# Performance work log

Hardware: AMD Instinct MI355X
Metric: run time of the kernel (lower is better)

The kernel has to match this reference:

```python
import jax, jax.numpy as jnp
import numpy as np

N_NODES = 16000
N_EDGES = 256000
DIM = 256
HEADS = 8
DH = DIM // HEADS
BLOCKS = 3
EPS = 1e-5


def _ln_graph(x, g, b):
    # PyG LayerNorm, mode='graph', batch=None: scalar mean/std over ALL elements,
    # then per-channel affine.
    x = x - x.mean()
    x = x / (x.std() + EPS)
    return x * g + b


def _block(x, src, dst, x_edge, inv_dist, p):
    (Wq, bq, Wk, bk, Wv, bv, We, Ws, bs, g1, b1, W1, c1, W2, c2, g2, b2) = p
    # per-edge gather + projections  [E, H, DH]
    q = (x[dst] @ Wq + bq).reshape(N_EDGES, HEADS, DH)
    e = (x_edge @ We).reshape(N_EDGES, HEADS, DH)          # lin_edge (no bias)
    k = (x[src] @ Wk + bk).reshape(N_EDGES, HEADS, DH) + e
    # distance-scaled attention logits [E, H]
    alpha = (q * k).sum(-1) * (inv_dist[:, None] / np.sqrt(DH))
    # segment softmax over destination nodes (PyG softmax, +1e-16 in denom)
    amax = jax.ops.segment_max(alpha, dst, num_segments=N_NODES)
    ex = jnp.exp(alpha - amax[dst])
    denom = jax.ops.segment_sum(ex, dst, num_segments=N_NODES)
    attn = ex / (denom[dst] + 1e-16)
    v = (x[src] @ Wv + bv).reshape(N_EDGES, HEADS, DH) + e
    msg = (v * attn[:, :, None]).reshape(N_EDGES, DIM)      # concat heads
    out = jax.ops.segment_sum(msg, dst, num_segments=N_NODES)
    out = out + x @ Ws + bs                                 # root / skip weight
    x = _ln_graph(x + out, g1, b1)                          # mha residual + norm
    ffn = jnp.maximum(x @ W1 + c1, 0.0) @ W2 + c2           # 2-layer ReLU MLP
    return _ln_graph(x + ffn, g2, b2)


def setup_inputs() -> dict:
    key = jax.random.key(0)
    ks = jax.random.split(key, 16)
    s = 0.05
    B = BLOCKS

    def w(k, shape):
        return jax.random.normal(k, shape, jnp.float32) * s

    return {
        'x': jax.random.normal(ks[0], (N_NODES, DIM), jnp.float32),
        'edge_index': jax.random.randint(ks[1], (2, N_EDGES), 0, N_NODES),
        'x_edge': jax.random.normal(ks[2], (N_EDGES, DIM), jnp.float32),
        'x_dist': jax.random.uniform(ks[3], (N_EDGES,), jnp.float32, 1.0, 5.0),
        'Wq': w(ks[4], (B, DIM, DIM)), 'bq': jnp.zeros((B, DIM), jnp.float32),
        'Wk': w(ks[5], (B, DIM, DIM)), 'bk': jnp.zeros((B, DIM), jnp.float32),
        'Wv': w(ks[6], (B, DIM, DIM)), 'bv': jnp.zeros((B, DIM), jnp.float32),
        'We': w(ks[7], (B, DIM, DIM)),
        'Wskip': w(ks[8], (B, DIM, DIM)), 'bskip': jnp.zeros((B, DIM), jnp.float32),
        'ln1_g': jnp.ones((B, DIM), jnp.float32), 'ln1_b': jnp.zeros((B, DIM), jnp.float32),
        'W1': w(ks[9], (B, DIM, 4 * DIM)), 'bf1': jnp.zeros((B, 4 * DIM), jnp.float32),
        'W2': w(ks[10], (B, 4 * DIM, DIM)), 'bf2': jnp.zeros((B, DIM), jnp.float32),
        'ln2_g': jnp.ones((B, DIM), jnp.float32), 'ln2_b': jnp.zeros((B, DIM), jnp.float32),
    }


def reference(x, edge_index, x_edge, x_dist, Wq, bq, Wk, bk, Wv, bv, We,
              Wskip, bskip, ln1_g, ln1_b, W1, bf1, W2, bf2, ln2_g, ln2_b):
    src, dst = edge_index[0], edge_index[1]  # PyG: x_j = x[src], x_i = x[dst]
    inv_dist = 1.0 / x_dist
    for i in range(BLOCKS):
        p = (Wq[i], bq[i], Wk[i], bk[i], Wv[i], bv[i], We[i], Wskip[i], bskip[i],
             ln1_g[i], ln1_b[i], W1[i], bf1[i], W2[i], bf2[i], ln2_g[i], ln2_b[i])
        x = _block(x, src, dst, x_edge, inv_dist, p)
    return x
```

## Files before the change

### kernel.cpp

```cpp
#include <hip/hip_runtime.h>
#include <hip/hip_bf16.h>
#include <cstddef>

#define N_NODES 16000
#define N_EDGES 256000
#define DIM 256
#define HEADS 8
#define DFF 1024
#define LN_EPS 1e-5f
#define CNT ((float)((size_t)N_NODES * DIM))
#define RSDH 0.17677669529663687f

typedef __attribute__((ext_vector_type(8))) short short8;
typedef __attribute__((ext_vector_type(4))) float floatx4;

__device__ __forceinline__ float bf2f(unsigned int s) {
    return __uint_as_float(s << 16);
}

__device__ __forceinline__ float2 ln_ms(const float* __restrict__ s) {
    float mu = s[0] * (1.0f / CNT);
    float var = s[1] * (1.0f / CNT) - mu * mu;
    float2 r; r.x = mu; r.y = 1.0f / (sqrtf(fmaxf(var, 0.0f)) + LN_EPS);
    return r;
}

__device__ __forceinline__ void async16(const __hip_bfloat16* g, __hip_bfloat16* l) {
    __builtin_amdgcn_global_load_lds(
        (const __attribute__((address_space(1))) void*)g,
        (__attribute__((address_space(3))) void*)l, 16, 0, 0);
}

__device__ __forceinline__ void pack8(__hip_bfloat16* d, float4 a, float4 b) {
    union { short8 f; __hip_bfloat16 h[8]; } u;
    u.h[0] = __float2bfloat16(a.x); u.h[1] = __float2bfloat16(a.y);
    u.h[2] = __float2bfloat16(a.z); u.h[3] = __float2bfloat16(a.w);
    u.h[4] = __float2bfloat16(b.x); u.h[5] = __float2bfloat16(b.y);
    u.h[6] = __float2bfloat16(b.z); u.h[7] = __float2bfloat16(b.w);
    *(short8*)d = u.f;
}

template<int BIAS, int RELU, int RES, int OBF16, int ACVT>
__global__ __launch_bounds__(256) void mgemm_k(
    const void* __restrict__ Ap, const __hip_bfloat16* __restrict__ Bt,
    const float* __restrict__ bias, const float* __restrict__ res,
    void* __restrict__ C, int M, int K, int N,
    const float* __restrict__ lnA_s, const float* __restrict__ lnA_g,
    const float* __restrict__ lnA_b,
    const float* __restrict__ lnR_s, const float* __restrict__ lnR_g,
    const float* __restrict__ lnR_b,
    float* __restrict__ ostats)
{
    __shared__ __hip_bfloat16 As[128 * 32];
    __shared__ __hip_bfloat16 Bs[128 * 32];
    __shared__ float rs[8];
    const int tid = threadIdx.x;
    const int lane = tid & 63, wv = tid >> 6;
    const int wm = (wv & 1) * 64, wn = (wv >> 1) * 64;
    const int row0 = blockIdx.y * 128, col0 = blockIdx.x * 128;
    const int lr = tid >> 2;
    const int lk = (tid & 3) * 8;

    float muA = 0.0f, scA = 1.0f;
    if (ACVT && lnA_s) { float2 t = ln_ms(lnA_s); muA = t.x; scA = t.y; }

    floatx4 acc[4][4];
    const floatx4 zf = {0.f, 0.f, 0.f, 0.f};
    #pragma unroll
    for (int i = 0; i < 4; i++)
        #pragma unroll
        for (int j = 0; j < 4; j++) acc[i][j] = zf;

    const int a_fo = (wm + (lane & 15)) * 32 + (lane >> 4) * 8;
    const int b_fo = (wn + (lane & 15)) * 32 + (lane >> 4) * 8;

    for (int k0 = 0; k0 < K; k0 += 32) {
        if (ACVT) {
            const float* A = (const float*)Ap;
            const float* p0 = A + (size_t)(row0 + lr) * K + k0 + lk;
            const float* p1 = A + (size_t)(row0 + lr + 64) * K + k0 + lk;
            float4 v0 = *(const float4*)(p0);
            float4 v1 = *(const float4*)(p0 + 4);
            float4 w0 = *(const float4*)(p1);
            float4 w1 = *(const float4*)(p1 + 4);
            if (lnA_s) {
                float4 ga = *(const float4*)(lnA_g + k0 + lk);
                float4 gb = *(const float4*)(lnA_g + k0 + lk + 4);
                float4 ba = *(const float4*)(lnA_b + k0 + lk);
                float4 bb = *(const float4*)(lnA_b + k0 + lk + 4);
                v0.x = (v0.x - muA) * scA * ga.x + ba.x;
                v0.y = (v0.y - muA) * scA * ga.y + ba.y;
                v0.z = (v0.z - muA) * scA * ga.z + ba.z;
                v0.w = (v0.w - muA) * scA * ga.w + ba.w;
                v1.x = (v1.x - muA) * scA * gb.x + bb.x;
                v1.y = (v1.y - muA) * scA * gb.y + bb.y;
                v1.z = (v1.z - muA) * scA * gb.z + bb.z;
                v1.w = (v1.w - muA) * scA * gb.w + bb.w;
                w0.x = (w0.x - muA) * scA * ga.x + ba.x;
                w0.y = (w0.y - muA) * scA * ga.y + ba.y;
                w0.z = (w0.z - muA) * scA * ga.z + ba.z;
                w0.w = (w0.w - muA) * scA * ga.w + ba.w;
                w1.x = (w1.x - muA) * scA * gb.x + bb.x;
                w1.y = (w1.y - muA) * scA * gb.y + bb.y;
                w1.z = (w1.z - muA) * scA * gb.z + bb.z;
                w1.w = (w1.w - muA) * scA * gb.w + bb.w;
            }
            pack8(As + tid * 8, v0, v1);
            pack8(As + 2048 + tid * 8, w0, w1);
        } else {
            const __hip_bfloat16* A = (const __hip_bfloat16*)Ap;
            async16(A + (size_t)(row0 + lr) * K + k0 + lk, As + tid * 8);
            async16(A + (size_t)(row0 + lr + 64) * K + k0 + lk, As + 2048 + tid * 8);
        }
        async16(Bt + (size_t)(col0 + lr) * K + k0 + lk, Bs + tid * 8);
        async16(Bt + (size_t)(col0 + lr + 64) * K + k0 + lk, Bs + 2048 + tid * 8);
        __syncthreads();
        short8 a[4], b[4];
        #pragma unroll
        for (int i = 0; i < 4; i++) {
            a[i] = *(const short8*)(As + a_fo + i * 16 * 32);
            b[i] = *(const short8*)(Bs + b_fo + i * 16 * 32);
        }
        #pragma unroll
        for (int i = 0; i < 4; i++)
            #pragma unroll
            for (int j = 0; j < 4; j++)
                acc[i][j] = __builtin_amdgcn_mfma_f32_16x16x32_bf16(a[i], b[j], acc[i][j], 0, 0, 0);
        __syncthreads();
    }
    float muR = 0.0f, scR = 1.0f;
    if (RES && lnR_s) { float2 t = ln_ms(lnR_s); muR = t.x; scR = t.y; }
    const int rbase = row0 + wm + (lane >> 4) * 4;
    const int cbase = col0 + wn + (lane & 15);
    float s1 = 0.0f, s2 = 0.0f;
    #pragma unroll
    for (int j = 0; j < 4; j++) {
        const int c = cbase + j * 16;
        float bb = BIAS ? bias[c] : 0.0f;
        float gr = (RES && lnR_s) ? lnR_g[c] : 1.0f;
        float br = (RES && lnR_s) ? lnR_b[c] : 0.0f;
        #pragma unroll
        for (int i = 0; i < 4; i++) {
            #pragma unroll
            for (int r = 0; r < 4; r++) {
                const int rr = rbase + i * 16 + r;
                float v = acc[i][j][r] + bb;
                if (RELU) v = fmaxf(v, 0.0f);
                if (RES) {
                    float rv = res[(size_t)rr * N + c];
                    if (lnR_s) rv = (rv - muR) * scR * gr + br;
                    v += rv;
                }
                if (ostats) { s1 += v; s2 += v * v; }
                if (OBF16) ((__hip_bfloat16*)C)[(size_t)rr * N + c] = __float2bfloat16(v);
                else       ((float*)C)[(size_t)rr * N + c] = v;
            }
        }
    }
    if (ostats) {
        #pragma unroll
        for (int o = 32; o > 0; o >>= 1) {
            s1 += __shfl_down(s1, o);
            s2 += __shfl_down(s2, o);
        }
        if (lane == 0) { rs[wv] = s1; rs[4 + wv] = s2; }
        __syncthreads();
        if (tid == 0) {
            atomicAdd(&ostats[0], rs[0] + rs[1] + rs[2] + rs[3]);
            atomicAdd(&ostats[1], rs[4] + rs[5] + rs[6] + rs[7]);
        }
    }
}

__global__ __launch_bounds__(256) void tcvt_k(const float* __restrict__ src,
                                              __hip_bfloat16* __restrict__ dst,
                                              int R, int C)
{
    __shared__ float t[32][33];
    const int c0 = blockIdx.x * 32, r0 = blockIdx.y * 32;
    const int tx = threadIdx.x & 31, ty = threadIdx.x >> 5;
    #pragma unroll
    for (int j = 0; j < 32; j += 8)
        t[ty + j][tx] = src[(size_t)(r0 + ty + j) * C + c0 + tx];
    __syncthreads();
    #pragma unroll
    for (int j = 0; j < 32; j += 8)
        dst[(size_t)(c0 + ty + j) * R + r0 + tx] = __float2bfloat16(t[tx][ty + j]);
}

__global__ __launch_bounds__(256) void bcat_k(const float* __restrict__ bq,
                                              const float* __restrict__ bk,
                                              const float* __restrict__ bv,
                                              const float* __restrict__ bs,
                                              float* __restrict__ o)
{
    int t = blockIdx.x * 256 + threadIdx.x;
    float v = (t < 256) ? bq[t] : (t < 512) ? bk[t - 256]
            : (t < 768) ? bv[t - 512] : bs[t - 768];
    o[t] = v;
}

__global__ __launch_bounds__(256) void hist_k(const int* __restrict__ dst, int* __restrict__ deg)
{
    int e = blockIdx.x * blockDim.x + threadIdx.x;
    if (e < N_EDGES) atomicAdd(&deg[dst[e]], 1);
}

__global__ __launch_bounds__(1024) void scan_k(const int* __restrict__ deg,
                                               int* __restrict__ rowptr,
                                               int* __restrict__ cursor)
{
    __shared__ int wsum[16];
    const int t = threadIdx.x;
    const int base = t * 16;
    int local[16];
    int s = 0;
    if (t < 1000) {
        #pragma unroll
        for (int j = 0; j < 16; j++) { local[j] = s; s += deg[base + j]; }
    }
    const int lane = t & 63, w = t >> 6;
    int v = s;
    #pragma unroll
    for (int off = 1; off < 64; off <<= 1) {
        int u = __shfl_up(v, off);
        if (lane >= off) v += u;
    }
    if (lane == 63) wsum[w] = v;
    __syncthreads();
    if (t == 0) {
        int r = 0;
        #pragma unroll
        for (int i = 0; i < 16; i++) { int u = wsum[i]; wsum[i] = r; r += u; }
    }
    __syncthreads();
    const int excl = v - s + wsum[w];
    if (t < 1000) {
        #pragma unroll
        for (int j = 0; j < 16; j++) {
            rowptr[base + j] = excl + local[j];
            cursor[base + j] = excl + local[j];
        }
        if (t == 999) rowptr[16000] = excl + s;
    }
}

__global__ __launch_bounds__(256) void scatter_k(const int* __restrict__ dst,
                                                 const int* __restrict__ src,
                                                 const float* __restrict__ xd,
                                                 int* __restrict__ cursor,
                                                 int* __restrict__ eperm,
                                                 int* __restrict__ srcp,
                                                 float* __restrict__ scale)
{
    int e = blockIdx.x * blockDim.x + threadIdx.x;
    if (e < N_EDGES) {
        int pos = atomicAdd(&cursor[dst[e]], 1);
        eperm[pos] = e;
        srcp[pos] = src[e];
        scale[pos] = RSDH / xd[e];
    }
}

__global__ __launch_bounds__(256) void eprep_k(const float* __restrict__ xe,
                                               const int* __restrict__ eperm,
                                               __hip_bfloat16* __restrict__ xeb)
{
    const int r = blockIdx.x * 4 + (threadIdx.x >> 6);
    const int lane = threadIdx.x & 63;
    const int e = eperm[r];
    float4 v = *(const float4*)(xe + (size_t)e * DIM + lane * 4);
    union { short4 s; __hip_bfloat16 h[4]; } u;
    u.h[0] = __float2bfloat16(v.x); u.h[1] = __float2bfloat16(v.y);
    u.h[2] = __float2bfloat16(v.z); u.h[3] = __float2bfloat16(v.w);
    *(short4*)(xeb + (size_t)r * DIM + lane * 4) = u.s;
}

__global__ __launch_bounds__(256) void node_agg_k(
    const float* __restrict__ qkvs, const __hip_bfloat16* __restrict__ Ep,
    const int* __restrict__ srcp, const float* __restrict__ scale,
    const int* __restrict__ rowptr,
    const float* __restrict__ xsrc, const float* __restrict__ lnx_s,
    const float* __restrict__ lnx_g, const float* __restrict__ lnx_b,
    float* __restrict__ y, float* __restrict__ ostats)
{
    __shared__ float rs[8];
    const int lane = threadIdx.x & 63;
    const int wv = threadIdx.x >> 6;
    const int n = blockIdx.x * 4 + wv;
    const float4 q = *(const float4*)(qkvs + (size_t)n * 1024 + lane * 4);
    float a0 = 0, a1 = 0, a2 = 0, a3 = 0, den = 0;
    const int beg = rowptr[n], end = rowptr[n + 1];
    int s = (beg < end) ? srcp[beg] : 0;
    for (int i = beg; i < end; i++) {
        const int scur = s;
        if (i + 1 < end) s = srcp[i + 1];
        const float sc = scale[i];
        const float4 kv = *(const float4*)(qkvs + (size_t)scur * 1024 + 256 + lane * 4);
        const float4 vv = *(const float4*)(qkvs + (size_t)scur * 1024 + 512 + lane * 4);
        const uint2 eb = *(const uint2*)(Ep + (size_t)i * DIM + lane * 4);
        const float e0 = bf2f(eb.x & 0xffffu), e1 = bf2f(eb.x >> 16);
        const float e2 = bf2f(eb.y & 0xffffu), e3 = bf2f(eb.y >> 16);
        float part = q.x * (kv.x + e0) + q.y * (kv.y + e1)
                   + q.z * (kv.z + e2) + q.w * (kv.w + e3);
        part += __shfl_xor(part, 1);
        part += __shfl_xor(part, 2);
        part += __shfl_xor(part, 4);
        const float ex = __expf(part * sc);
        den += ex;
        a0 = fmaf(vv.x + e0, ex, a0);
        a1 = fmaf(vv.y + e1, ex, a1);
        a2 = fmaf(vv.z + e2, ex, a2);
        a3 = fmaf(vv.w + e3, ex, a3);
    }
    const float dn = 1.0f / (den + 1e-16f);
    const size_t o = (size_t)n * DIM + lane * 4;
    float4 xr = *(const float4*)(xsrc + o);
    if (lnx_s) {
        float2 t = ln_ms(lnx_s);
        const float4 g4 = *(const float4*)(lnx_g + lane * 4);
        const float4 b4 = *(const float4*)(lnx_b + lane * 4);
        xr.x = (xr.x - t.x) * t.y * g4.x + b4.x;
        xr.y = (xr.y - t.x) * t.y * g4.y + b4.y;
        xr.z = (xr.z - t.x) * t.y * g4.z + b4.z;
        xr.w = (xr.w - t.x) * t.y * g4.w + b4.w;
    }
    const float4 sr = *(const float4*)(qkvs + (size_t)n * 1024 + 768 + lane * 4);
    float4 out;
    out.x = xr.x + a0 * dn + sr.x;
    out.y = xr.y + a1 * dn + sr.y;
    out.z = xr.z + a2 * dn + sr.z;
    out.w = xr.w + a3 * dn + sr.w;
    *(float4*)(y + o) = out;
    float s1 = out.x + out.y + out.z + out.w;
    float s2 = out.x * out.x + out.y * out.y + out.z * out.z + out.w * out.w;
    #pragma unroll
    for (int of = 32; of > 0; of >>= 1) {
        s1 += __shfl_down(s1, of);
        s2 += __shfl_down(s2, of);
    }
    if (lane == 0) { rs[wv] = s1; rs[4 + wv] = s2; }
    __syncthreads();
    if (threadIdx.x == 0) {
        atomicAdd(&ostats[0], rs[0] + rs[1] + rs[2] + rs[3]);
        atomicAdd(&ostats[1], rs[4] + rs[5] + rs[6] + rs[7]);
    }
}

__global__ __launch_bounds__(256) void apply_k(
    const float* __restrict__ y, const float* __restrict__ stats,
    const float* __restrict__ g, const float* __restrict__ b,
    float* __restrict__ xo)
{
    int idx = blockIdx.x * blockDim.x + threadIdx.x;
    float2 t = ln_ms(stats);
    int cb = (idx & 63) * 4;
    float4 v  = *(const float4*)(y + (size_t)idx * 4);
    float4 gv = *(const float4*)(g + cb);
    float4 bv = *(const float4*)(b + cb);
    float4 o;
    o.x = (v.x - t.x) * t.y * gv.x + bv.x;
    o.y = (v.y - t.x) * t.y * gv.y + bv.y;
    o.z = (v.z - t.x) * t.y * gv.z + bv.z;
    o.w = (v.w - t.x) * t.y * gv.w + bv.w;
    *(float4*)(xo + (size_t)idx * 4) = o;
}

extern "C" void kernel_launch(void* const* d_in, const int* in_sizes, int n_in,
                              void* d_out, int out_size, void* d_ws, size_t ws_size,
                              hipStream_t stream) {
    const float* x_in   = (const float*)d_in[0];
    const int*   ei     = (const int*)d_in[1];
    const int*   src    = ei;
    const int*   dstp   = ei + N_EDGES;
    const float* x_edge = (const float*)d_in[2];
    const float* x_dist = (const float*)d_in[3];
    const float* Wq  = (const float*)d_in[4];
    const float* bq  = (const float*)d_in[5];
    const float* Wk  = (const float*)d_in[6];
    const float* bk  = (const float*)d_in[7];
    const float* Wv  = (const float*)d_in[8];
    const float* bv  = (const float*)d_in[9];
    const float* We  = (const float*)d_in[10];
    const float* Wsk = (const float*)d_in[11];
    const float* bsk = (const float*)d_in[12];
    const float* g1  = (const float*)d_in[13];
    const float* b1  = (const float*)d_in[14];
    const float* W1  = (const float*)d_in[15];
    const float* c1  = (const float*)d_in[16];
    const float* W2  = (const float*)d_in[17];
    const float* c2  = (const float*)d_in[18];
    const float* g2  = (const float*)d_in[19];
    const float* b2  = (const float*)d_in[20];

    char* p = (char*)d_ws;
    float* ybuf = (float*)p; p += (size_t)N_NODES * DIM * sizeof(float);
    float* qkvs = (float*)p; p += (size_t)N_NODES * 1024 * sizeof(float);
    __hip_bfloat16* hb16 = (__hip_bfloat16*)p; p += (size_t)N_NODES * 1024 * 2;
    __hip_bfloat16* Ep   = (__hip_bfloat16*)p; p += (size_t)N_EDGES * DIM * 2;
    __hip_bfloat16* xeb  = (__hip_bfloat16*)p; p += (size_t)N_EDGES * DIM * 2;
    __hip_bfloat16* WqkvsT = (__hip_bfloat16*)p; p += (size_t)3 * 1024 * 256 * 2;
    __hip_bfloat16* WeT    = (__hip_bfloat16*)p; p += (size_t)3 * 256 * 256 * 2;
    __hip_bfloat16* W1T    = (__hip_bfloat16*)p; p += (size_t)3 * 1024 * 256 * 2;
    __hip_bfloat16* W2T    = (__hip_bfloat16*)p; p += (size_t)3 * 256 * 1024 * 2;
    float* bqkvs = (float*)p; p += (size_t)3 * 1024 * sizeof(float);
    float* stats = (float*)p;  p += 64;
    int* deg     = (int*)p;    p += (size_t)N_NODES * sizeof(int);
    int* rowptr  = (int*)p;    p += (size_t)(N_NODES + 4) * sizeof(int);
    int* cursor  = (int*)p;    p += (size_t)N_NODES * sizeof(int);
    int* eperm   = (int*)p;    p += (size_t)N_EDGES * sizeof(int);
    int* srcp    = (int*)p;    p += (size_t)N_EDGES * sizeof(int);
    float* scale = (float*)p;  p += (size_t)N_EDGES * sizeof(float);

    const dim3 blk(256);

    hipMemsetAsync(deg, 0, (size_t)N_NODES * sizeof(int), stream);
    hipMemsetAsync(stats, 0, 48, stream);
    hist_k<<<N_EDGES / 256, blk, 0, stream>>>(dstp, deg);
    scan_k<<<1, 1024, 0, stream>>>(deg, rowptr, cursor);
    scatter_k<<<N_EDGES / 256, blk, 0, stream>>>(dstp, src, x_dist, cursor, eperm, srcp, scale);
    eprep_k<<<N_EDGES / 4, blk, 0, stream>>>(x_edge, eperm, xeb);

    for (int i = 0; i < 3; i++) {
        const float* wsrc[4] = {Wq, Wk, Wv, Wsk};
        for (int c = 0; c < 4; c++)
            tcvt_k<<<dim3(8, 8), blk, 0, stream>>>(wsrc[c] + (size_t)i * 65536,
                WqkvsT + (size_t)i * 262144 + (size_t)c * 65536, 256, 256);
        tcvt_k<<<dim3(8, 8), blk, 0, stream>>>(We + (size_t)i * 65536,
                WeT + (size_t)i * 65536, 256, 256);
        tcvt_k<<<dim3(32, 8), blk, 0, stream>>>(W1 + (size_t)i * 262144,
                W1T + (size_t)i * 262144, 256, 1024);
        tcvt_k<<<dim3(8, 32), blk, 0, stream>>>(W2 + (size_t)i * 262144,
                W2T + (size_t)i * 262144, 1024, 256);
        bcat_k<<<4, blk, 0, stream>>>(bq + (size_t)i * 256, bk + (size_t)i * 256,
                bv + (size_t)i * 256, bsk + (size_t)i * 256, bqkvs + (size_t)i * 1024);
    }

    for (int i = 0; i < 3; i++) {
        const size_t bo = (size_t)i * DIM;
        const size_t b1o = (size_t)i * DFF;
        float* ln1 = stats + (size_t)i * 4;
        float* ln2 = stats + (size_t)i * 4 + 2;
        const float* pls = (i == 0) ? nullptr : stats + (size_t)(i - 1) * 4 + 2;
        const float* plg = (i == 0) ? nullptr : g2 + (size_t)(i - 1) * 256;
        const float* plb = (i == 0) ? nullptr : b2 + (size_t)(i - 1) * 256;
        const float* xsrc = (i == 0) ? x_in : ybuf;

        mgemm_k<1,0,0,0,1><<<dim3(8, 125), blk, 0, stream>>>(
            xsrc, WqkvsT + (size_t)i * 262144, bqkvs + (size_t)i * 1024, nullptr,
            qkvs, N_NODES, DIM, 1024, pls, plg, plb, nullptr, nullptr, nullptr, nullptr);
        mgemm_k<0,0,0,1,0><<<dim3(2, 2000), blk, 0, stream>>>(
            xeb, WeT + (size_t)i * 65536, nullptr, nullptr,
            Ep, N_EDGES, DIM, DIM, nullptr, nullptr, nullptr, nullptr, nullptr, nullptr, nullptr);
        node_agg_k<<<N_NODES / 4, blk, 0, stream>>>(qkvs, Ep, srcp, scale, rowptr,
                                                    xsrc, pls, plg, plb, ybuf, ln1);
        mgemm_k<1,1,0,1,1><<<dim3(8, 125), blk, 0, stream>>>(
            ybuf, W1T + (size_t)i * 262144, c1 + b1o, nullptr,
            hb16, N_NODES, DIM, DFF, ln1, g1 + bo, b1 + bo, nullptr, nullptr, nullptr, nullptr);
        mgemm_k<1,0,1,0,0><<<dim3(2, 125), blk, 0, stream>>>(
            hb16, W2T + (size_t)i * 262144, c2 + bo, ybuf,
            ybuf, N_NODES, DFF, DIM, nullptr, nullptr, nullptr, ln1, g1 + bo, b1 + bo, ln2);
        if (i == 2)
            apply_k<<<(N_NODES * DIM) / 1024, blk, 0, stream>>>(
                ybuf, ln2, g2 + bo, b2 + bo, (float*)d_out);
    }
}
```

Measured before the change: 1.611 ms.

## Store K/V projections as interleaved bf16 and prefetch next edge in aggregation

The fused QKVS projection is split into two GEMMs: Q and skip stay fp32, while K and V are written as bf16 interleaved per lane so one 16-byte load fetches both K and V for four channels. The node aggregation loop now software-prefetches the next edge's K/V, edge projection and scale before computing the current one. This is meant to cut the gather traffic over 256K random source rows and hide its latency, at the cost of bf16 rounding on K and V and an extra GEMM launch that reads the input twice.

```diff
diff --git a/kernel.cpp b/kernel.cpp
--- a/kernel.cpp
+++ b/kernel.cpp
@@ -152,8 +152,15 @@
                     v += rv;
                 }
                 if (ostats) { s1 += v; s2 += v * v; }
-                if (OBF16) ((__hip_bfloat16*)C)[(size_t)rr * N + c] = __float2bfloat16(v);
-                else       ((float*)C)[(size_t)rr * N + c] = v;
+                if (OBF16 == 2) {
+                    const int cc = c & 255;
+                    const int idx = ((cc >> 2) << 3) + (cc & 3) + ((c >> 8) << 2);
+                    ((__hip_bfloat16*)C)[(size_t)rr * N + idx] = __float2bfloat16(v);
+                } else if (OBF16) {
+                    ((__hip_bfloat16*)C)[(size_t)rr * N + c] = __float2bfloat16(v);
+                } else {
+                    ((float*)C)[(size_t)rr * N + c] = v;
+                }
             }
         }
     }
@@ -188,15 +195,15 @@
         dst[(size_t)(c0 + ty + j) * R + r0 + tx] = __float2bfloat16(t[tx][ty + j]);
 }
 
-__global__ __launch_bounds__(256) void bcat_k(const float* __restrict__ bq,
-                                              const float* __restrict__ bk,
-                                              const float* __restrict__ bv,
-                                              const float* __restrict__ bs,
+__global__ __launch_bounds__(256) void bcat_k(const float* __restrict__ ba,
+                                              const float* __restrict__ bb,
+                                              const float* __restrict__ bc,
+                                              const float* __restrict__ bd,
                                               float* __restrict__ o)
 {
     int t = blockIdx.x * 256 + threadIdx.x;
-    float v = (t < 256) ? bq[t] : (t < 512) ? bk[t - 256]
-            : (t < 768) ? bv[t - 512] : bs[t - 768];
+    float v = (t < 256) ? ba[t] : (t < 512) ? bb[t - 256]
+            : (t < 768) ? bc[t - 512] : bd[t - 768];
     o[t] = v;
 }
 
@@ -277,7 +284,8 @@
 }
 
 __global__ __launch_bounds__(256) void node_agg_k(
-    const float* __restrict__ qkvs, const __hip_bfloat16* __restrict__ Ep,
+    const float* __restrict__ qs, const __hip_bfloat16* __restrict__ kvb,
+    const __hip_bfloat16* __restrict__ Ep,
     const int* __restrict__ srcp, const float* __restrict__ scale,
     const int* __restrict__ rowptr,
     const float* __restrict__ xsrc, const float* __restrict__ lnx_s,
@@ -288,30 +296,41 @@
     const int lane = threadIdx.x & 63;
     const int wv = threadIdx.x >> 6;
     const int n = blockIdx.x * 4 + wv;
-    const float4 q = *(const float4*)(qkvs + (size_t)n * 1024 + lane * 4);
+    const float4 q = *(const float4*)(qs + (size_t)n * 512 + lane * 4);
     float a0 = 0, a1 = 0, a2 = 0, a3 = 0, den = 0;
     const int beg = rowptr[n], end = rowptr[n + 1];
-    int s = (beg < end) ? srcp[beg] : 0;
+    uint4 kvn = {0, 0, 0, 0}; uint2 ebn = {0, 0}; float scn = 0.0f;
+    int spf = 0;
+    if (beg < end) {
+        const int s0 = srcp[beg];
+        spf = (beg + 1 < end) ? srcp[beg + 1] : 0;
+        kvn = *(const uint4*)(kvb + (size_t)s0 * 512 + lane * 8);
+        ebn = *(const uint2*)(Ep + (size_t)beg * DIM + lane * 4);
+        scn = scale[beg];
+    }
     for (int i = beg; i < end; i++) {
-        const int scur = s;
-        if (i + 1 < end) s = srcp[i + 1];
-        const float sc = scale[i];
-        const float4 kv = *(const float4*)(qkvs + (size_t)scur * 1024 + 256 + lane * 4);
-        const float4 vv = *(const float4*)(qkvs + (size_t)scur * 1024 + 512 + lane * 4);
-        const uint2 eb = *(const uint2*)(Ep + (size_t)i * DIM + lane * 4);
+        const uint4 kv = kvn; const uint2 eb = ebn; const float sc = scn;
+        if (i + 1 < end) {
+            kvn = *(const uint4*)(kvb + (size_t)spf * 512 + lane * 8);
+            ebn = *(const uint2*)(Ep + (size_t)(i + 1) * DIM + lane * 4);
+            scn = scale[i + 1];
+            spf = (i + 2 < end) ? srcp[i + 2] : 0;
+        }
         const float e0 = bf2f(eb.x & 0xffffu), e1 = bf2f(eb.x >> 16);
         const float e2 = bf2f(eb.y & 0xffffu), e3 = bf2f(eb.y >> 16);
-        float part = q.x * (kv.x + e0) + q.y * (kv.y + e1)
-                   + q.z * (kv.z + e2) + q.w * (kv.w + e3);
+        float part = q.x * (bf2f(kv.x & 0xffffu) + e0)
+                   + q.y * (bf2f(kv.x >> 16) + e1)
+                   + q.z * (bf2f(kv.y & 0xffffu) + e2)
+                   + q.w * (bf2f(kv.y >> 16) + e3);
         part += __shfl_xor(part, 1);
         part += __shfl_xor(part, 2);
         part += __shfl_xor(part, 4);
         const float ex = __expf(part * sc);
         den += ex;
-        a0 = fmaf(vv.x + e0, ex, a0);
-        a1 = fmaf(vv.y + e1, ex, a1);
-        a2 = fmaf(vv.z + e2, ex, a2);
-        a3 = fmaf(vv.w + e3, ex, a3);
+        a0 = fmaf(bf2f(kv.z & 0xffffu) + e0, ex, a0);
+        a1 = fmaf(bf2f(kv.z >> 16) + e1, ex, a1);
+        a2 = fmaf(bf2f(kv.w & 0xffffu) + e2, ex, a2);
+        a3 = fmaf(bf2f(kv.w >> 16) + e3, ex, a3);
     }
     const float dn = 1.0f / (den + 1e-16f);
     const size_t o = (size_t)n * DIM + lane * 4;
@@ -325,7 +344,7 @@
         xr.z = (xr.z - t.x) * t.y * g4.z + b4.z;
         xr.w = (xr.w - t.x) * t.y * g4.w + b4.w;
     }
-    const float4 sr = *(const float4*)(qkvs + (size_t)n * 1024 + 768 + lane * 4);
+    const float4 sr = *(const float4*)(qs + (size_t)n * 512 + 256 + lane * 4);
     float4 out;
     out.x = xr.x + a0 * dn + sr.x;
     out.y = xr.y + a1 * dn + sr.y;
@@ -395,7 +414,8 @@
 
     char* p = (char*)d_ws;
     float* ybuf = (float*)p; p += (size_t)N_NODES * DIM * sizeof(float);
-    float* qkvs = (float*)p; p += (size_t)N_NODES * 1024 * sizeof(float);
+    float* qsb  = (float*)p; p += (size_t)N_NODES * 512 * sizeof(float);
+    __hip_bfloat16* kvb = (__hip_bfloat16*)p; p += (size_t)N_NODES * 512 * 2;
     __hip_bfloat16* hb16 = (__hip_bfloat16*)p; p += (size_t)N_NODES * 1024 * 2;
     __hip_bfloat16* Ep   = (__hip_bfloat16*)p; p += (size_t)N_EDGES * DIM * 2;
     __hip_bfloat16* xeb  = (__hip_bfloat16*)p; p += (size_t)N_EDGES * DIM * 2;
@@ -422,7 +442,7 @@
     eprep_k<<<N_EDGES / 4, blk, 0, stream>>>(x_edge, eperm, xeb);
 
     for (int i = 0; i < 3; i++) {
-        const float* wsrc[4] = {Wq, Wk, Wv, Wsk};
+        const float* wsrc[4] = {Wq, Wsk, Wk, Wv};
         for (int c = 0; c < 4; c++)
             tcvt_k<<<dim3(8, 8), blk, 0, stream>>>(wsrc[c] + (size_t)i * 65536,
                 WqkvsT + (size_t)i * 262144 + (size_t)c * 65536, 256, 256);
@@ -432,8 +452,8 @@
                 W1T + (size_t)i * 262144, 256, 1024);
         tcvt_k<<<dim3(8, 32), blk, 0, stream>>>(W2 + (size_t)i * 262144,
                 W2T + (size_t)i * 262144, 1024, 256);
-        bcat_k<<<4, blk, 0, stream>>>(bq + (size_t)i * 256, bk + (size_t)i * 256,
-                bv + (size_t)i * 256, bsk + (size_t)i * 256, bqkvs + (size_t)i * 1024);
+        bcat_k<<<4, blk, 0, stream>>>(bq + (size_t)i * 256, bsk + (size_t)i * 256,
+                bk + (size_t)i * 256, bv + (size_t)i * 256, bqkvs + (size_t)i * 1024);
     }
 
     for (int i = 0; i < 3; i++) {
@@ -446,13 +466,16 @@
         const float* plb = (i == 0) ? nullptr : b2 + (size_t)(i - 1) * 256;
         const float* xsrc = (i == 0) ? x_in : ybuf;
 
-        mgemm_k<1,0,0,0,1><<<dim3(8, 125), blk, 0, stream>>>(
+        mgemm_k<1,0,0,0,1><<<dim3(4, 125), blk, 0, stream>>>(
             xsrc, WqkvsT + (size_t)i * 262144, bqkvs + (size_t)i * 1024, nullptr,
-            qkvs, N_NODES, DIM, 1024, pls, plg, plb, nullptr, nullptr, nullptr, nullptr);
+            qsb, N_NODES, DIM, 512, pls, plg, plb, nullptr, nullptr, nullptr, nullptr);
+        mgemm_k<1,0,0,2,1><<<dim3(4, 125), blk, 0, stream>>>(
+            xsrc, WqkvsT + (size_t)i * 262144 + 131072, bqkvs + (size_t)i * 1024 + 512, nullptr,
+            kvb, N_NODES, DIM, 512, pls, plg, plb, nullptr, nullptr, nullptr, nullptr);
         mgemm_k<0,0,0,1,0><<<dim3(2, 2000), blk, 0, stream>>>(
             xeb, WeT + (size_t)i * 65536, nullptr, nullptr,
             Ep, N_EDGES, DIM, DIM, nullptr, nullptr, nullptr, nullptr, nullptr, nullptr, nullptr);
-        node_agg_k<<<N_NODES / 4, blk, 0, stream>>>(qkvs, Ep, srcp, scale, rowptr,
+        node_agg_k<<<N_NODES / 4, blk, 0, stream>>>(qsb, kvb, Ep, srcp, scale, rowptr,
                                                     xsrc, pls, plg, plb, ybuf, ln1);
         mgemm_k<1,1,0,1,1><<<dim3(8, 125), blk, 0, stream>>>(
             ybuf, W1T + (size_t)i * 262144, c1 + b1o, nullptr,
```

New measurement: 1.570 ms. -2.6%, faster.
